# Kernel tuning notes

Hardware: AMD Instinct MI355X
Metric: run time of the kernel (lower is better)

Reference implementation:

```python
import jax, jax.numpy as jnp
import numpy as np

N = 50000        # nodes
E = 800000       # edges (avg degree 16)
F_IN = 128       # in_channels
HID = 32         # hidden_channels per head
H = 8            # heads
DH = HID * H     # 256, concat dim
NC = {'TL': 12, 'YL': 30, 'TS': 60, 'TZ': 120}
NEG_SLOPE = 0.2  # PyG GATConv default


def setup_inputs() -> dict:
    key = jax.random.key(0)
    ks = jax.random.split(key, 40)
    rn = lambda k, s, sc=0.1: jax.random.normal(k, s, jnp.float32) * sc
    inp = {}
    inp['x'] = jax.random.normal(ks[0], (N, F_IN), jnp.float32)
    inp['edge_index'] = jax.random.randint(ks[1], (2, E), 0, N, dtype=jnp.int64)
    # conv1: in -> H x HID (concat)
    inp['W1'] = rn(ks[2], (F_IN, DH)); inp['a1s'] = rn(ks[3], (H, HID)); inp['a1d'] = rn(ks[4], (H, HID)); inp['b1'] = jnp.zeros((DH,), jnp.float32)
    # conv2: DH -> H x HID (concat)
    inp['W2'] = rn(ks[5], (DH, DH)); inp['a2s'] = rn(ks[6], (H, HID)); inp['a2d'] = rn(ks[7], (H, HID)); inp['b2'] = jnp.zeros((DH,), jnp.float32)
    # task heads: DH -> C, heads=1, concat=False
    i = 8
    for t, c in NC.items():
        inp['W_' + t] = rn(ks[i], (DH, c)); i += 1
        inp['as_' + t] = rn(ks[i], (1, c)); i += 1
        inp['ad_' + t] = rn(ks[i], (1, c)); i += 1
        inp['b_' + t] = jnp.zeros((c,), jnp.float32)
    return inp


def gat_conv(x, src, dst, W, a_s, a_d, b, concat):
    """PyG-style GATConv (eval mode, self-loops already in src/dst)."""
    n = x.shape[0]
    heads, out_ch = a_s.shape
    h = (x @ W).reshape(n, heads, out_ch)                 # [N,H,C]
    alpha_s = jnp.einsum('nhc,hc->nh', h, a_s)            # [N,H]
    alpha_d = jnp.einsum('nhc,hc->nh', h, a_d)
    e = jax.nn.leaky_relu(alpha_s[src] + alpha_d[dst], NEG_SLOPE)   # [E,H]
    # numerically-stable segment softmax over incoming edges of each dst
    m = jax.ops.segment_max(e, dst, num_segments=n)
    ex = jnp.exp(e - m[dst])
    denom = jax.ops.segment_sum(ex, dst, num_segments=n)
    alpha = ex / (denom[dst] + 1e-16)                     # [E,H]
    out = jax.ops.segment_sum(alpha[:, :, None] * h[src], dst, num_segments=n)  # [N,H,C]
    out = out.reshape(n, heads * out_ch) if concat else out.mean(axis=1)
    return out + b


def reference(x, edge_index, W1, a1s, a1d, b1, W2, a2s, a2d, b2,
              W_TL, as_TL, ad_TL, b_TL, W_YL, as_YL, ad_YL, b_YL,
              W_TS, as_TS, ad_TS, b_TS, W_TZ, as_TZ, ad_TZ, b_TZ):
    n = x.shape[0]
    loop = jnp.arange(n, dtype=edge_index.dtype)
    src = jnp.concatenate([edge_index[0], loop])
    dst = jnp.concatenate([edge_index[1], loop])
    h = jax.nn.elu(gat_conv(x, src, dst, W1, a1s, a1d, b1, True))
    h = gat_conv(h, src, dst, W2, a2s, a2d, b2, True)
    tl = jax.nn.log_softmax(gat_conv(h, src, dst, W_TL, as_TL, ad_TL, b_TL, False), axis=1)
    yl = jax.nn.log_softmax(gat_conv(h, src, dst, W_YL, as_YL, ad_YL, b_YL, False), axis=1)
    ts = jax.nn.log_softmax(gat_conv(h, src, dst, W_TS, as_TS, ad_TS, b_TS, False), axis=1)
    tz = jax.nn.log_softmax(gat_conv(h, src, dst, W_TZ, as_TZ, ad_TZ, b_TZ, False), axis=1)
    return (tl, yl, ts, tz)
```

## Files before the change

### kernel.cpp

```cpp
#include <hip/hip_runtime.h>
#include <math.h>


#define NEG_SLOPE 0.2f

typedef short s8v __attribute__((ext_vector_type(8)));
typedef short s4v __attribute__((ext_vector_type(4)));
typedef float f4v __attribute__((ext_vector_type(4)));

__device__ __forceinline__ short f2bf(float x) {
    unsigned u = __float_as_uint(x);
    u += 0x7fffu + ((u >> 16) & 1u);
    return (short)(u >> 16);
}
__device__ __forceinline__ float bf2f(short b) {
    return __uint_as_float(((unsigned)(unsigned short)b) << 16);
}
__device__ __forceinline__ void split2(float x, short& h, short& l) {
    h = f2bf(x);
    l = f2bf(x - bf2f(h));
}
__device__ __forceinline__ float4 bf4_to_f4(s4v v) {
    return make_float4(bf2f(v[0]), bf2f(v[1]), bf2f(v[2]), bf2f(v[3]));
}
__device__ __forceinline__ float leaky(float x) {
    return fmaxf(x, NEG_SLOPE * x);
}


__global__ void init_kernel(int* __restrict__ deg, int* __restrict__ cursor, int n) {
    int i = blockIdx.x * blockDim.x + threadIdx.x;
    if (i < n) { deg[i] = 1; cursor[i] = 0; }
}

__global__ void count_kernel(const int* __restrict__ dst, int* __restrict__ deg, int E) {
    int i = blockIdx.x * blockDim.x + threadIdx.x;
    if (i < E) atomicAdd(&deg[dst[i]], 1);
}

__global__ __launch_bounds__(1024) void scan_kernel(const int* __restrict__ deg,
                                                    int* __restrict__ rowstart, int n) {
    __shared__ int wsum[16];
    __shared__ int carry_sh;
    int lane = threadIdx.x & 63, wv = threadIdx.x >> 6;
    if (threadIdx.x == 0) { carry_sh = 0; rowstart[0] = 0; }
    __syncthreads();
    for (int base = 0; base < n; base += 8192) {
        int vals[8];
        int sum = 0;
        int i0 = base + threadIdx.x * 8;
        #pragma unroll
        for (int j = 0; j < 8; ++j) {
            int i = i0 + j;
            int v = (i < n) ? ((deg[i] + 3) & ~3) : 0;
            sum += v;
            vals[j] = sum;
        }
        int incl = sum;
        #pragma unroll
        for (int off = 1; off < 64; off <<= 1) {
            int t = __shfl_up(incl, off);
            if (lane >= off) incl += t;
        }
        if (lane == 63) wsum[wv] = incl;
        __syncthreads();
        if (wv == 0) {
            int s = (lane < 16) ? wsum[lane] : 0;
            #pragma unroll
            for (int off = 1; off < 16; off <<= 1) {
                int t = __shfl_up(s, off);
                if (lane >= off) s += t;
            }
            if (lane < 16) wsum[lane] = s;
        }
        __syncthreads();
        int wexcl = (wv == 0) ? 0 : wsum[wv - 1];
        int excl = carry_sh + wexcl + (incl - sum);
        #pragma unroll
        for (int j = 0; j < 8; ++j) {
            int i = i0 + j;
            if (i < n) rowstart[i + 1] = excl + vals[j];
        }
        __syncthreads();
        if (threadIdx.x == 0) carry_sh += wsum[15];
        __syncthreads();
    }
}

__global__ void scatter_kernel(const int* __restrict__ src, const int* __restrict__ dst,
                               const int* __restrict__ rowstart, int* __restrict__ cursor,
                               int* __restrict__ csr, int E, int n) {
    int i = blockIdx.x * blockDim.x + threadIdx.x;
    if (i >= E + n) return;
    int s, d;
    if (i < E) { s = src[i]; d = dst[i]; }
    else       { s = d = i - E; }
    int p = atomicAdd(&cursor[d], 1);
    csr[rowstart[d] + p] = s;
}


__global__ void tobf_kernel(const float* __restrict__ A, short* __restrict__ Ah, int n4) {
    int i = blockIdx.x * blockDim.x + threadIdx.x;
    if (i >= n4) return;
    float4 v = ((const float4*)A)[i];
    s4v hv = {f2bf(v.x), f2bf(v.y), f2bf(v.z), f2bf(v.w)};
    ((s4v*)Ah)[i] = hv;
}

__global__ void split_bt_kernel(const float* __restrict__ B, short* __restrict__ Bh,
                                short* __restrict__ Bl, int K, int Nc, int kshift) {
    int idx = blockIdx.x * blockDim.x + threadIdx.x;
    if (idx >= Nc * K) return;
    int n = idx >> kshift;
    int k = idx & (K - 1);
    float v = B[(size_t)k * Nc + n];
    short h, l; split2(v, h, l);
    Bh[idx] = h;
    Bl[idx] = l;
}

__global__ void fold_alpha8_kernel(const float* __restrict__ W,
                                   const float* __restrict__ a_s, const float* __restrict__ a_d,
                                   short* __restrict__ Bth, short* __restrict__ Btl,
                                   int K, int Nfeat) {
    int idx = blockIdx.x * blockDim.x + threadIdx.x;
    if (idx >= K * 16) return;
    int j = idx / K, k = idx % K;
    int h = j & 7;
    const float* av = ((j < 8) ? a_s : a_d) + h * 32;
    const float* wp = W + (size_t)k * 256 + h * 32;
    float s = 0.f;
    #pragma unroll
    for (int c = 0; c < 32; ++c) s += wp[c] * av[c];
    short hi, lo; split2(s, hi, lo);
    size_t off = (size_t)(Nfeat + j) * K + k;
    Bth[off] = hi; Btl[off] = lo;
}

__global__ void fold_alpha4_kernel(const float* __restrict__ Wcat,
                                   const float* __restrict__ ascat, const float* __restrict__ adcat,
                                   short* __restrict__ Bth, short* __restrict__ Btl) {
    int idx = blockIdx.x * blockDim.x + threadIdx.x;
    if (idx >= 256 * 8) return;
    int j = idx >> 8, k = idx & 255;
    const int CO[4] = {0, 12, 44, 104};
    const int CL[4] = {12, 32, 60, 120};
    int t = j & 3;
    const float* av = ((j < 4) ? ascat : adcat) + CO[t];
    const float* wp = Wcat + (size_t)k * 224 + CO[t];
    float s = 0.f;
    for (int c = 0; c < CL[t]; ++c) s += wp[c] * av[c];
    short hi, lo; split2(s, hi, lo);
    size_t off = (size_t)(224 + j) * 256 + k;
    Bth[off] = hi; Btl[off] = lo;
}


#define MB 128
#define NB 64
#define KS 32

__global__ __launch_bounds__(256) void gemm_mfma_kernel(
        const short* __restrict__ Ah_g,
        const short* __restrict__ Bth_g, const short* __restrict__ Btl_g,
        short* __restrict__ Cb, int cb_stride,
        float* __restrict__ als, float* __restrict__ ald, int nsplit,
        int M, int K, int Nfeat, int NcExt) {
    __shared__ __align__(16) short Ah[MB][40];
    __shared__ __align__(16) short Bh[NB][40];
    __shared__ __align__(16) short Bl[NB][40];

    int t = threadIdx.x;
    int lane = t & 63, w = t >> 6;
    int quad = lane >> 4, l16 = lane & 15;
    int row0 = blockIdx.y * MB, col0 = blockIdx.x * NB;

    f4v acc[2][4];
    #pragma unroll
    for (int mt = 0; mt < 2; ++mt)
        #pragma unroll
        for (int nt = 0; nt < 4; ++nt)
            acc[mt][nt] = (f4v){0.f, 0.f, 0.f, 0.f};

    for (int k0 = 0; k0 < K; k0 += KS) {
        __syncthreads();
        #pragma unroll
        for (int i = 0; i < 2; ++i) {
            int u = i * 256 + t;
            int r = u >> 2, kk = (u & 3) * 8;
            int gr = row0 + r;
            s8v vh = {0, 0, 0, 0, 0, 0, 0, 0};
            if (gr < M) vh = *(const s8v*)(Ah_g + (size_t)gr * K + k0 + kk);
            *(s8v*)&Ah[r][kk] = vh;
        }
        {
            int n = t >> 2, kk = (t & 3) * 8;
            int gc = col0 + n;
            s8v vh = {0, 0, 0, 0, 0, 0, 0, 0};
            s8v vl = {0, 0, 0, 0, 0, 0, 0, 0};
            if (gc < NcExt) {
                vh = *(const s8v*)(Bth_g + (size_t)gc * K + k0 + kk);
                vl = *(const s8v*)(Btl_g + (size_t)gc * K + k0 + kk);
            }
            *(s8v*)&Bh[n][kk] = vh;
            *(s8v*)&Bl[n][kk] = vl;
        }
        __syncthreads();

        int kb = quad * 8;
        s8v a_f[2], b_h[4], b_l[4];
        #pragma unroll
        for (int mt = 0; mt < 2; ++mt) {
            int r = w * 32 + mt * 16 + l16;
            a_f[mt] = *(const s8v*)&Ah[r][kb];
        }
        #pragma unroll
        for (int nt = 0; nt < 4; ++nt) {
            int c = nt * 16 + l16;
            b_h[nt] = *(const s8v*)&Bh[c][kb];
            b_l[nt] = *(const s8v*)&Bl[c][kb];
        }
        #pragma unroll
        for (int mt = 0; mt < 2; ++mt)
            #pragma unroll
            for (int nt = 0; nt < 4; ++nt) {
                acc[mt][nt] = __builtin_amdgcn_mfma_f32_16x16x32_bf16(
                    a_f[mt], b_h[nt], acc[mt][nt], 0, 0, 0);
                acc[mt][nt] = __builtin_amdgcn_mfma_f32_16x16x32_bf16(
                    a_f[mt], b_l[nt], acc[mt][nt], 0, 0, 0);
            }
    }

    #pragma unroll
    for (int mt = 0; mt < 2; ++mt) {
        #pragma unroll
        for (int nt = 0; nt < 4; ++nt) {
            int gc = col0 + nt * 16 + l16;
            if (gc >= NcExt) continue;
            #pragma unroll
            for (int r = 0; r < 4; ++r) {
                int gr = row0 + w * 32 + mt * 16 + quad * 4 + r;
                if (gr >= M) continue;
                float v = acc[mt][nt][r];
                if (gc < Nfeat) {
                    Cb[(size_t)gr * cb_stride + gc] = f2bf(v);
                } else {
                    int j = gc - Nfeat;
                    if (j < nsplit)            als[(size_t)gr * nsplit + j] = v;
                    else if (j < 2 * nsplit)   ald[(size_t)gr * nsplit + (j - nsplit)] = v;
                }
            }
        }
    }
}


__global__ __launch_bounds__(256) void gat_gather_kernel(
        const short* __restrict__ hb,
        const float* __restrict__ als, const float* __restrict__ ald,
        const int* __restrict__ rowstart, const int* __restrict__ csr,
        const float* __restrict__ bias, short* __restrict__ oh, int n, int elu) {
    int wid  = blockIdx.x * 4 + (threadIdx.x >> 6);
    int lane = threadIdx.x & 63;
    if (wid >= n) return;
    int row = rowstart[wid];
    int pdeg = rowstart[wid + 1] - row;
    int hp = lane >> 3;
    int ch = lane * 4;
    int ph = lane & 7;
    const int* cp = csr + row;
    float aldv = ald[(size_t)wid * 8 + ph];

    float4 acc = {0.f, 0.f, 0.f, 0.f};
    float wsum = 0.f;
    for (int base = 0; base < pdeg; base += 64) {
        int cnt = min(pdeg - base, 64);
        int idxv = -1;
        if (lane < cnt) idxv = cp[base + lane];
        int e = 0;
        for (; e + 8 <= cnt; e += 8) {
            int si[8];
            #pragma unroll
            for (int i = 0; i < 8; ++i) {
                int r = __builtin_amdgcn_readlane(idxv, e + i);
                si[i] = r < 0 ? 0 : r;
            }
            s4v hv[8];
            #pragma unroll
            for (int i = 0; i < 8; ++i)
                hv[i] = *(const s4v*)(hb + (size_t)si[i] * 256 + ch);
            int sprod = __shfl(idxv, e + (lane >> 3));
            int sp = sprod < 0 ? 0 : sprod;
            float wall = __expf(leaky(als[(size_t)sp * 8 + ph] + aldv));
            if (sprod < 0) wall = 0.f;
            float w[8];
            #pragma unroll
            for (int i = 0; i < 8; ++i) w[i] = __shfl(wall, i * 8 + hp);
            #pragma unroll
            for (int i = 0; i < 8; ++i) {
                float4 h = bf4_to_f4(hv[i]);
                acc.x += w[i] * h.x; acc.y += w[i] * h.y;
                acc.z += w[i] * h.z; acc.w += w[i] * h.w;
                wsum += w[i];
            }
        }
        if (e < cnt) {
            int si[4];
            #pragma unroll
            for (int i = 0; i < 4; ++i) {
                int r = __builtin_amdgcn_readlane(idxv, e + i);
                si[i] = r < 0 ? 0 : r;
            }
            s4v hv[4];
            #pragma unroll
            for (int i = 0; i < 4; ++i)
                hv[i] = *(const s4v*)(hb + (size_t)si[i] * 256 + ch);
            int sprod = __shfl(idxv, e + ((lane >> 3) & 3));
            int sp = sprod < 0 ? 0 : sprod;
            float wall = __expf(leaky(als[(size_t)sp * 8 + ph] + aldv));
            if (sprod < 0) wall = 0.f;
            float w[4];
            #pragma unroll
            for (int i = 0; i < 4; ++i) w[i] = __shfl(wall, i * 8 + hp);
            #pragma unroll
            for (int i = 0; i < 4; ++i) {
                float4 h = bf4_to_f4(hv[i]);
                acc.x += w[i] * h.x; acc.y += w[i] * h.y;
                acc.z += w[i] * h.z; acc.w += w[i] * h.w;
                wsum += w[i];
            }
        }
    }
    float inv = 1.f / (wsum + 1e-16f);
    float4 b4 = *(const float4*)(bias + ch);
    float v[4] = {acc.x * inv + b4.x, acc.y * inv + b4.y,
                  acc.z * inv + b4.z, acc.w * inv + b4.w};
    if (elu) {
        #pragma unroll
        for (int j = 0; j < 4; ++j)
            v[j] = (v[j] > 0.f) ? v[j] : __expf(v[j]) - 1.f;
    }
    s4v hvo = {f2bf(v[0]), f2bf(v[1]), f2bf(v[2]), f2bf(v[3])};
    *(s4v*)(oh + (size_t)wid * 256 + ch) = hvo;
}


__global__ void pack_w_kernel(const float* __restrict__ wTL, const float* __restrict__ wYL,
                              const float* __restrict__ wTS, const float* __restrict__ wTZ,
                              const float* __restrict__ bTL, const float* __restrict__ bYL,
                              const float* __restrict__ bTS, const float* __restrict__ bTZ,
                              const float* __restrict__ asTL, const float* __restrict__ asYL,
                              const float* __restrict__ asTS, const float* __restrict__ asTZ,
                              const float* __restrict__ adTL, const float* __restrict__ adYL,
                              const float* __restrict__ adTS, const float* __restrict__ adTZ,
                              float* __restrict__ Wcat, float* __restrict__ bcat,
                              float* __restrict__ ascat, float* __restrict__ adcat) {
    int idx = blockIdx.x * blockDim.x + threadIdx.x;
    if (idx < 256 * 224) {
        int r = idx / 224, c = idx % 224;
        float v = 0.f;
        if (c < 12)       v = wTL[r * 12 + c];
        else if (c < 42)  v = wYL[r * 30 + (c - 12)];
        else if (c < 44)  v = 0.f;
        else if (c < 104) v = wTS[r * 60 + (c - 44)];
        else              v = wTZ[r * 120 + (c - 104)];
        Wcat[idx] = v;
    }
    if (idx < 224) {
        float b = 0.f, as_ = 0.f, ad_ = 0.f;
        if (idx < 12)       { b = bTL[idx];       as_ = asTL[idx];       ad_ = adTL[idx]; }
        else if (idx < 42)  { b = bYL[idx - 12];  as_ = asYL[idx - 12];  ad_ = adYL[idx - 12]; }
        else if (idx < 44)  { }
        else if (idx < 104) { b = bTS[idx - 44];  as_ = asTS[idx - 44];  ad_ = adTS[idx - 44]; }
        else                { b = bTZ[idx - 104]; as_ = asTZ[idx - 104]; ad_ = adTZ[idx - 104]; }
        bcat[idx]  = b;
        ascat[idx] = as_;
        adcat[idx] = ad_;
    }
}


__device__ __forceinline__ float sel4(int t, float v0, float v1, float v2, float v3) {
    return (t == 0) ? v0 : (t == 1) ? v1 : (t == 2) ? v2 : v3;
}

__global__ __launch_bounds__(256) void task_gather_ls_kernel(
        const short* __restrict__ htb,
        const float* __restrict__ ast, const float* __restrict__ adt,
        const int* __restrict__ rowstart, const int* __restrict__ csr,
        const float* __restrict__ bcat, float* __restrict__ out, int n) {
    int wid  = blockIdx.x * 4 + (threadIdx.x >> 6);
    int lane = threadIdx.x & 63;
    if (wid >= n) return;
    int row = rowstart[wid];
    int pdeg = rowstart[wid + 1] - row;
    int ch0 = (lane < 56) ? lane * 4 : 0;
    int t = (lane < 3) ? 0 : (lane < 11) ? 1 : (lane < 26) ? 2 : 3;
    int pt = lane & 3;
    int COp = (t == 0) ? 0 : (t == 1) ? 12 : (t == 2) ? 44 : 104;
    int COr = (t == 0) ? 0 : (t == 1) ? 12 : (t == 2) ? 42 : 102;
    int CLr = (t == 0) ? 12 : (t == 1) ? 30 : (t == 2) ? 60 : 120;
    bool valj[4];
    #pragma unroll
    for (int j = 0; j < 4; ++j)
        valj[j] = (unsigned)(ch0 + j - COp) < (unsigned)CLr;

    const int* cp = csr + row;
    float adtv = adt[(size_t)wid * 4 + pt];

    float acc[4] = {0.f, 0.f, 0.f, 0.f};
    float wsv = 0.f;
    for (int base = 0; base < pdeg; base += 64) {
        int cnt = min(pdeg - base, 64);
        int idxv = -1;
        if (lane < cnt) idxv = cp[base + lane];
        int e = 0;
        for (; e + 8 <= cnt; e += 8) {
            int si[8];
            #pragma unroll
            for (int i = 0; i < 8; ++i) {
                int r = __builtin_amdgcn_readlane(idxv, e + i);
                si[i] = r < 0 ? 0 : r;
            }
            s4v hv[8];
            #pragma unroll
            for (int i = 0; i < 8; ++i)
                hv[i] = *(const s4v*)(htb + (size_t)si[i] * 224 + ch0);
            int sprod = __shfl(idxv, e + (lane >> 3));
            int sp = sprod < 0 ? 0 : sprod;
            float wall = __expf(leaky(ast[(size_t)sp * 4 + pt] + adtv));
            if (sprod < 0) wall = 0.f;
            float w[8];
            #pragma unroll
            for (int i = 0; i < 8; ++i) w[i] = __shfl(wall, i * 8 + t);
            #pragma unroll
            for (int i = 0; i < 8; ++i) {
                float4 h = bf4_to_f4(hv[i]);
                acc[0] += w[i] * h.x; acc[1] += w[i] * h.y;
                acc[2] += w[i] * h.z; acc[3] += w[i] * h.w;
                wsv += w[i];
            }
        }
        if (e < cnt) {
            int si[4];
            #pragma unroll
            for (int i = 0; i < 4; ++i) {
                int r = __builtin_amdgcn_readlane(idxv, e + i);
                si[i] = r < 0 ? 0 : r;
            }
            s4v hv[4];
            #pragma unroll
            for (int i = 0; i < 4; ++i)
                hv[i] = *(const s4v*)(htb + (size_t)si[i] * 224 + ch0);
            int sprod = __shfl(idxv, e + ((lane >> 3) & 3));
            int sp = sprod < 0 ? 0 : sprod;
            float wall = __expf(leaky(ast[(size_t)sp * 4 + pt] + adtv));
            if (sprod < 0) wall = 0.f;
            float w[4];
            #pragma unroll
            for (int i = 0; i < 4; ++i) w[i] = __shfl(wall, i * 8 + t);
            #pragma unroll
            for (int i = 0; i < 4; ++i) {
                float4 h = bf4_to_f4(hv[i]);
                acc[0] += w[i] * h.x; acc[1] += w[i] * h.y;
                acc[2] += w[i] * h.z; acc[3] += w[i] * h.w;
                wsv += w[i];
            }
        }
    }
    float inv = 1.f / (wsv + 1e-16f);

    float vout[4];
    float m = -1e30f;
    #pragma unroll
    for (int j = 0; j < 4; ++j) {
        float v = 0.f;
        if (valj[j]) { v = acc[j] * inv + bcat[ch0 + j]; m = fmaxf(m, v); }
        vout[j] = v;
    }
    float m0 = (t == 0) ? m : -1e30f;
    float m1 = (t == 1) ? m : -1e30f;
    float m2 = (t == 2) ? m : -1e30f;
    float m3 = (t == 3) ? m : -1e30f;
    #pragma unroll
    for (int off = 1; off < 64; off <<= 1) {
        m0 = fmaxf(m0, __shfl_xor(m0, off));
        m1 = fmaxf(m1, __shfl_xor(m1, off));
        m2 = fmaxf(m2, __shfl_xor(m2, off));
        m3 = fmaxf(m3, __shfl_xor(m3, off));
    }
    float mt = sel4(t, m0, m1, m2, m3);
    float sacc = 0.f;
    #pragma unroll
    for (int j = 0; j < 4; ++j)
        if (valj[j]) sacc += __expf(vout[j] - mt);
    float s0 = (t == 0) ? sacc : 0.f;
    float s1 = (t == 1) ? sacc : 0.f;
    float s2 = (t == 2) ? sacc : 0.f;
    float s3 = (t == 3) ? sacc : 0.f;
    #pragma unroll
    for (int off = 1; off < 64; off <<= 1) {
        s0 += __shfl_xor(s0, off);
        s1 += __shfl_xor(s1, off);
        s2 += __shfl_xor(s2, off);
        s3 += __shfl_xor(s3, off);
    }
    float st = sel4(t, s0, s1, s2, s3);
    float lse = mt + __logf(st);
    #pragma unroll
    for (int j = 0; j < 4; ++j)
        if (valj[j])
            out[(size_t)COr * n + (size_t)wid * CLr + (ch0 + j - COp)] = vout[j] - lse;
}


extern "C" void kernel_launch(void* const* d_in, const int* in_sizes, int n_in,
                              void* d_out, int out_size, void* d_ws, size_t ws_size,
                              hipStream_t stream) {
    const float* x   = (const float*)d_in[0];
    const int*   ei  = (const int*)d_in[1];
    const float* W1  = (const float*)d_in[2];
    const float* a1s = (const float*)d_in[3];
    const float* a1d = (const float*)d_in[4];
    const float* b1  = (const float*)d_in[5];
    const float* W2  = (const float*)d_in[6];
    const float* a2s = (const float*)d_in[7];
    const float* a2d = (const float*)d_in[8];
    const float* b2  = (const float*)d_in[9];
    const float* W_TL = (const float*)d_in[10]; const float* as_TL = (const float*)d_in[11];
    const float* ad_TL = (const float*)d_in[12]; const float* b_TL = (const float*)d_in[13];
    const float* W_YL = (const float*)d_in[14]; const float* as_YL = (const float*)d_in[15];
    const float* ad_YL = (const float*)d_in[16]; const float* b_YL = (const float*)d_in[17];
    const float* W_TS = (const float*)d_in[18]; const float* as_TS = (const float*)d_in[19];
    const float* ad_TS = (const float*)d_in[20]; const float* b_TS = (const float*)d_in[21];
    const float* W_TZ = (const float*)d_in[22]; const float* as_TZ = (const float*)d_in[23];
    const float* ad_TZ = (const float*)d_in[24]; const float* b_TZ = (const float*)d_in[25];

    const int N = in_sizes[0] / 128;
    const int E = in_sizes[1] / 2;
    const int* e_src = ei;
    const int* e_dst = ei + E;
    const int M4 = E + 4 * N;

    float* ws = (float*)d_ws;
    float* B1   = ws;
    float* B2   = B1 + (size_t)N * 256;
    float* B3   = B2 + (size_t)N * 256;
    float* as1  = B3 + (size_t)N * 256;
    float* ad1  = as1 + (size_t)N * 8;
    float* as2  = ad1 + (size_t)N * 8;
    float* ad2  = as2 + (size_t)N * 8;
    float* ast  = ad2 + (size_t)N * 8;
    float* adt  = ast + (size_t)N * 4;
    float* Wcat = adt + (size_t)N * 4;
    float* bcat = Wcat + 256 * 224;
    float* ascat = bcat + 224;
    float* adcat = ascat + 224;
    int* deg      = (int*)(adcat + 224);
    int* rowstart = deg + N;
    int* cursor   = rowstart + (N + 4);
    int* csr      = cursor + N;
    uintptr_t wsp = (uintptr_t)(csr + M4);
    wsp = (wsp + 15) & ~(uintptr_t)15;
    short* W1h = (short*)wsp;
    short* W1l = W1h + 272 * 128;
    short* W2h = W1l + 272 * 128;
    short* W2l = W2h + 272 * 256;
    short* Wth = W2l + 272 * 256;
    short* Wtl = Wth + 232 * 256;
    short* Xh  = (short*)B1;
    short* Sh  = (short*)B1;
    short* Th  = (short*)B1;
    short* h1b = (short*)B2;
    short* h2b = (short*)B2;
    short* htb = (short*)B2;

    float* out = (float*)d_out;

    const int B = 256;
    init_kernel<<<(N + B - 1) / B, B, 0, stream>>>(deg, cursor, N);
    count_kernel<<<(E + B - 1) / B, B, 0, stream>>>(e_dst, deg, E);
    scan_kernel<<<1, 1024, 0, stream>>>(deg, rowstart, N);
    hipMemsetAsync(csr, 0xFF, (size_t)M4 * sizeof(int), stream);
    scatter_kernel<<<(E + N + B - 1) / B, B, 0, stream>>>(e_src, e_dst, rowstart, cursor, csr, E, N);
    pack_w_kernel<<<(256 * 224 + B - 1) / B, B, 0, stream>>>(W_TL, W_YL, W_TS, W_TZ,
        b_TL, b_YL, b_TS, b_TZ, as_TL, as_YL, as_TS, as_TZ, ad_TL, ad_YL, ad_TS, ad_TZ,
        Wcat, bcat, ascat, adcat);
    split_bt_kernel<<<(256 * 128 + B - 1) / B, B, 0, stream>>>(W1, W1h, W1l, 128, 256, 7);
    split_bt_kernel<<<(256 * 256 + B - 1) / B, B, 0, stream>>>(W2, W2h, W2l, 256, 256, 8);
    split_bt_kernel<<<(224 * 256 + B - 1) / B, B, 0, stream>>>(Wcat, Wth, Wtl, 256, 224, 8);
    fold_alpha8_kernel<<<(128 * 16 + B - 1) / B, B, 0, stream>>>(W1, a1s, a1d, W1h, W1l, 128, 256);
    fold_alpha8_kernel<<<(256 * 16 + B - 1) / B, B, 0, stream>>>(W2, a2s, a2d, W2h, W2l, 256, 256);
    fold_alpha4_kernel<<<(256 * 8 + B - 1) / B, B, 0, stream>>>(Wcat, ascat, adcat, Wth, Wtl);
    tobf_kernel<<<((N * 128 / 4) + B - 1) / B, B, 0, stream>>>(x, Xh, N * 128 / 4);
    {
        dim3 g((272 + NB - 1) / NB, (N + MB - 1) / MB);
        gemm_mfma_kernel<<<g, 256, 0, stream>>>(Xh, W1h, W1l, h1b, 256,
                                                as1, ad1, 8, N, 128, 256, 272);
    }
    gat_gather_kernel<<<(N + 3) / 4, 256, 0, stream>>>(h1b, as1, ad1, rowstart, csr, b1, Sh, N, 1);
    {
        dim3 g((272 + NB - 1) / NB, (N + MB - 1) / MB);
        gemm_mfma_kernel<<<g, 256, 0, stream>>>(Sh, W2h, W2l, h2b, 256,
                                                as2, ad2, 8, N, 256, 256, 272);
    }
    gat_gather_kernel<<<(N + 3) / 4, 256, 0, stream>>>(h2b, as2, ad2, rowstart, csr, b2, Th, N, 0);
    {
        dim3 g((232 + NB - 1) / NB, (N + MB - 1) / MB);
        gemm_mfma_kernel<<<g, 256, 0, stream>>>(Th, Wth, Wtl, htb, 224,
                                                ast, adt, 4, N, 256, 224, 232);
    }
    task_gather_ls_kernel<<<(N + 3) / 4, 256, 0, stream>>>(htb, ast, adt, rowstart, csr, bcat, out, N);
}
```

Baseline: 595.2 us.

## Use 16-byte row loads in gather kernels, split edges across half-waves

Both gather kernels now have each lane load 8 bf16 features (16 bytes) rather than 4. The two half-waves each handle alternate edges, and their partial sums are combined at the end with a cross-lane shuffle. To let the task-head gather use aligned 8-wide loads, the concatenated task weights are re-laid out with each head starting on an 8-aligned column, and the intermediate buffer uses a 256 stride. The intent is fewer, wider memory transactions and more edges in flight per wave. The cost is the final reduction and half the lanes sitting idle in the epilogue.

```diff
diff --git a/kernel.cpp b/kernel.cpp
--- a/kernel.cpp
+++ b/kernel.cpp
@@ -19,9 +19,6 @@
 __device__ __forceinline__ void split2(float x, short& h, short& l) {
     h = f2bf(x);
     l = f2bf(x - bf2f(h));
-}
-__device__ __forceinline__ float4 bf4_to_f4(s4v v) {
-    return make_float4(bf2f(v[0]), bf2f(v[1]), bf2f(v[2]), bf2f(v[3]));
 }
 __device__ __forceinline__ float leaky(float x) {
     return fmaxf(x, NEG_SLOPE * x);
@@ -144,15 +141,15 @@
     int idx = blockIdx.x * blockDim.x + threadIdx.x;
     if (idx >= 256 * 8) return;
     int j = idx >> 8, k = idx & 255;
-    const int CO[4] = {0, 12, 44, 104};
-    const int CL[4] = {12, 32, 60, 120};
+    const int CO[4] = {0, 16, 48, 112};
+    const int CL[4] = {12, 30, 60, 120};
     int t = j & 3;
     const float* av = ((j < 4) ? ascat : adcat) + CO[t];
-    const float* wp = Wcat + (size_t)k * 224 + CO[t];
+    const float* wp = Wcat + (size_t)k * 232 + CO[t];
     float s = 0.f;
     for (int c = 0; c < CL[t]; ++c) s += wp[c] * av[c];
     short hi, lo; split2(s, hi, lo);
-    size_t off = (size_t)(224 + j) * 256 + k;
+    size_t off = (size_t)(232 + j) * 256 + k;
     Bth[off] = hi; Btl[off] = lo;
 }
 
@@ -266,13 +263,15 @@
     if (wid >= n) return;
     int row = rowstart[wid];
     int pdeg = rowstart[wid + 1] - row;
-    int hp = lane >> 3;
-    int ch = lane * 4;
-    int ph = lane & 7;
+    int ep  = lane >> 5;
+    int cb  = lane & 31;
+    int ch8 = cb * 8;
+    int hd  = cb >> 2;
+    int ph  = lane & 7;
     const int* cp = csr + row;
     float aldv = ald[(size_t)wid * 8 + ph];
 
-    float4 acc = {0.f, 0.f, 0.f, 0.f};
+    float acc[8] = {0.f, 0.f, 0.f, 0.f, 0.f, 0.f, 0.f, 0.f};
     float wsum = 0.f;
     for (int base = 0; base < pdeg; base += 64) {
         int cnt = min(pdeg - base, 64);
@@ -280,69 +279,77 @@
         if (lane < cnt) idxv = cp[base + lane];
         int e = 0;
         for (; e + 8 <= cnt; e += 8) {
-            int si[8];
-            #pragma unroll
-            for (int i = 0; i < 8; ++i) {
-                int r = __builtin_amdgcn_readlane(idxv, e + i);
-                si[i] = r < 0 ? 0 : r;
-            }
-            s4v hv[8];
-            #pragma unroll
-            for (int i = 0; i < 8; ++i)
-                hv[i] = *(const s4v*)(hb + (size_t)si[i] * 256 + ch);
+            int sg[8];
+            #pragma unroll
+            for (int g = 0; g < 8; ++g) {
+                int r = __builtin_amdgcn_readlane(idxv, e + g);
+                sg[g] = r < 0 ? 0 : r;
+            }
+            s8v hv[4];
+            #pragma unroll
+            for (int k = 0; k < 4; ++k) {
+                int ssel = ep ? sg[2 * k + 1] : sg[2 * k];
+                hv[k] = *(const s8v*)(hb + (size_t)ssel * 256 + ch8);
+            }
             int sprod = __shfl(idxv, e + (lane >> 3));
             int sp = sprod < 0 ? 0 : sprod;
             float wall = __expf(leaky(als[(size_t)sp * 8 + ph] + aldv));
             if (sprod < 0) wall = 0.f;
-            float w[8];
-            #pragma unroll
-            for (int i = 0; i < 8; ++i) w[i] = __shfl(wall, i * 8 + hp);
-            #pragma unroll
-            for (int i = 0; i < 8; ++i) {
-                float4 h = bf4_to_f4(hv[i]);
-                acc.x += w[i] * h.x; acc.y += w[i] * h.y;
-                acc.z += w[i] * h.z; acc.w += w[i] * h.w;
-                wsum += w[i];
+            #pragma unroll
+            for (int k = 0; k < 4; ++k) {
+                float wk = __shfl(wall, (2 * k + ep) * 8 + hd);
+                #pragma unroll
+                for (int j = 0; j < 8; ++j)
+                    acc[j] += wk * bf2f(hv[k][j]);
+                wsum += wk;
             }
         }
         if (e < cnt) {
-            int si[4];
-            #pragma unroll
-            for (int i = 0; i < 4; ++i) {
-                int r = __builtin_amdgcn_readlane(idxv, e + i);
-                si[i] = r < 0 ? 0 : r;
-            }
-            s4v hv[4];
-            #pragma unroll
-            for (int i = 0; i < 4; ++i)
-                hv[i] = *(const s4v*)(hb + (size_t)si[i] * 256 + ch);
+            int sg[4];
+            #pragma unroll
+            for (int g = 0; g < 4; ++g) {
+                int r = __builtin_amdgcn_readlane(idxv, e + g);
+                sg[g] = r < 0 ? 0 : r;
+            }
+            s8v hv[2];
+            #pragma unroll
+            for (int k = 0; k < 2; ++k) {
+                int ssel = ep ? sg[2 * k + 1] : sg[2 * k];
+                hv[k] = *(const s8v*)(hb + (size_t)ssel * 256 + ch8);
+            }
             int sprod = __shfl(idxv, e + ((lane >> 3) & 3));
             int sp = sprod < 0 ? 0 : sprod;
             float wall = __expf(leaky(als[(size_t)sp * 8 + ph] + aldv));
             if (sprod < 0) wall = 0.f;
-            float w[4];
-            #pragma unroll
-            for (int i = 0; i < 4; ++i) w[i] = __shfl(wall, i * 8 + hp);
-            #pragma unroll
-            for (int i = 0; i < 4; ++i) {
-                float4 h = bf4_to_f4(hv[i]);
-                acc.x += w[i] * h.x; acc.y += w[i] * h.y;
-                acc.z += w[i] * h.z; acc.w += w[i] * h.w;
-                wsum += w[i];
-            }
-        }
-    }
+            #pragma unroll
+            for (int k = 0; k < 2; ++k) {
+                float wk = __shfl(wall, (2 * k + ep) * 8 + hd);
+                #pragma unroll
+                for (int j = 0; j < 8; ++j)
+                    acc[j] += wk * bf2f(hv[k][j]);
+                wsum += wk;
+            }
+        }
+    }
+    wsum += __shfl_xor(wsum, 32);
+    #pragma unroll
+    for (int j = 0; j < 8; ++j)
+        acc[j] += __shfl_xor(acc[j], 32);
     float inv = 1.f / (wsum + 1e-16f);
-    float4 b4 = *(const float4*)(bias + ch);
-    float v[4] = {acc.x * inv + b4.x, acc.y * inv + b4.y,
-                  acc.z * inv + b4.z, acc.w * inv + b4.w};
-    if (elu) {
-        #pragma unroll
-        for (int j = 0; j < 4; ++j)
-            v[j] = (v[j] > 0.f) ? v[j] : __expf(v[j]) - 1.f;
-    }
-    s4v hvo = {f2bf(v[0]), f2bf(v[1]), f2bf(v[2]), f2bf(v[3])};
-    *(s4v*)(oh + (size_t)wid * 256 + ch) = hvo;
+    if (lane < 32) {
+        float4 b0 = *(const float4*)(bias + ch8);
+        float4 b1 = *(const float4*)(bias + ch8 + 4);
+        float bb[8] = {b0.x, b0.y, b0.z, b0.w, b1.x, b1.y, b1.z, b1.w};
+        short vv[8];
+        #pragma unroll
+        for (int j = 0; j < 8; ++j) {
+            float v = acc[j] * inv + bb[j];
+            if (elu) v = (v > 0.f) ? v : __expf(v) - 1.f;
+            vv[j] = f2bf(v);
+        }
+        s8v hvo = {vv[0], vv[1], vv[2], vv[3], vv[4], vv[5], vv[6], vv[7]};
+        *(s8v*)(oh + (size_t)wid * 256 + ch8) = hvo;
+    }
 }
 
 
@@ -357,23 +364,21 @@
                               float* __restrict__ Wcat, float* __restrict__ bcat,
                               float* __restrict__ ascat, float* __restrict__ adcat) {
     int idx = blockIdx.x * blockDim.x + threadIdx.x;
-    if (idx < 256 * 224) {
-        int r = idx / 224, c = idx % 224;
+    if (idx < 256 * 232) {
+        int r = idx / 232, c = idx % 232;
         float v = 0.f;
-        if (c < 12)       v = wTL[r * 12 + c];
-        else if (c < 42)  v = wYL[r * 30 + (c - 12)];
-        else if (c < 44)  v = 0.f;
-        else if (c < 104) v = wTS[r * 60 + (c - 44)];
-        else              v = wTZ[r * 120 + (c - 104)];
+        if (c < 12)                    v = wTL[r * 12 + c];
+        else if (c >= 16 && c < 46)    v = wYL[r * 30 + (c - 16)];
+        else if (c >= 48 && c < 108)   v = wTS[r * 60 + (c - 48)];
+        else if (c >= 112 && c < 232)  v = wTZ[r * 120 + (c - 112)];
         Wcat[idx] = v;
     }
-    if (idx < 224) {
+    if (idx < 232) {
         float b = 0.f, as_ = 0.f, ad_ = 0.f;
-        if (idx < 12)       { b = bTL[idx];       as_ = asTL[idx];       ad_ = adTL[idx]; }
-        else if (idx < 42)  { b = bYL[idx - 12];  as_ = asYL[idx - 12];  ad_ = adYL[idx - 12]; }
-        else if (idx < 44)  { }
-        else if (idx < 104) { b = bTS[idx - 44];  as_ = asTS[idx - 44];  ad_ = adTS[idx - 44]; }
-        else                { b = bTZ[idx - 104]; as_ = asTZ[idx - 104]; ad_ = adTZ[idx - 104]; }
+        if (idx < 12)                    { b = bTL[idx];       as_ = asTL[idx];       ad_ = adTL[idx]; }
+        else if (idx >= 16 && idx < 46)  { b = bYL[idx - 16];  as_ = asYL[idx - 16];  ad_ = adYL[idx - 16]; }
+        else if (idx >= 48 && idx < 108) { b = bTS[idx - 48];  as_ = asTS[idx - 48];  ad_ = adTS[idx - 48]; }
+        else if (idx >= 112)             { b = bTZ[idx - 112]; as_ = asTZ[idx - 112]; ad_ = adTZ[idx - 112]; }
         bcat[idx]  = b;
         ascat[idx] = as_;
         adcat[idx] = ad_;
@@ -395,21 +400,25 @@
     if (wid >= n) return;
     int row = rowstart[wid];
     int pdeg = rowstart[wid + 1] - row;
-    int ch0 = (lane < 56) ? lane * 4 : 0;
-    int t = (lane < 3) ? 0 : (lane < 11) ? 1 : (lane < 26) ? 2 : 3;
+    int ep  = lane >> 5;
+    int cb  = lane & 31;
+    int cbr = (cb <= 28) ? cb : 0;
+    int ch8 = cbr * 8;
+    int t = (ch8 >= 112) ? 3 : (ch8 >= 48) ? 2 : (ch8 >= 16) ? 1 : 0;
+    int pe = (lane & 31) >> 2;
     int pt = lane & 3;
-    int COp = (t == 0) ? 0 : (t == 1) ? 12 : (t == 2) ? 44 : 104;
+    int COp = (t == 0) ? 0 : (t == 1) ? 16 : (t == 2) ? 48 : 112;
     int COr = (t == 0) ? 0 : (t == 1) ? 12 : (t == 2) ? 42 : 102;
     int CLr = (t == 0) ? 12 : (t == 1) ? 30 : (t == 2) ? 60 : 120;
-    bool valj[4];
-    #pragma unroll
-    for (int j = 0; j < 4; ++j)
-        valj[j] = (unsigned)(ch0 + j - COp) < (unsigned)CLr;
+    bool valj[8];
+    #pragma unroll
+    for (int j = 0; j < 8; ++j)
+        valj[j] = (cb <= 28) && ((unsigned)(ch8 + j - COp) < (unsigned)CLr);
 
     const int* cp = csr + row;
     float adtv = adt[(size_t)wid * 4 + pt];
 
-    float acc[4] = {0.f, 0.f, 0.f, 0.f};
+    float acc[8] = {0.f, 0.f, 0.f, 0.f, 0.f, 0.f, 0.f, 0.f};
     float wsv = 0.f;
     for (int base = 0; base < pdeg; base += 64) {
         int cnt = min(pdeg - base, 64);
@@ -417,66 +426,73 @@
         if (lane < cnt) idxv = cp[base + lane];
         int e = 0;
         for (; e + 8 <= cnt; e += 8) {
-            int si[8];
-            #pragma unroll
-            for (int i = 0; i < 8; ++i) {
-                int r = __builtin_amdgcn_readlane(idxv, e + i);
-                si[i] = r < 0 ? 0 : r;
-            }
-            s4v hv[8];
-            #pragma unroll
-            for (int i = 0; i < 8; ++i)
-                hv[i] = *(const s4v*)(htb + (size_t)si[i] * 224 + ch0);
-            int sprod = __shfl(idxv, e + (lane >> 3));
+            int sg[8];
+            #pragma unroll
+            for (int g = 0; g < 8; ++g) {
+                int r = __builtin_amdgcn_readlane(idxv, e + g);
+                sg[g] = r < 0 ? 0 : r;
+            }
+            s8v hv[4];
+            #pragma unroll
+            for (int k = 0; k < 4; ++k) {
+                int ssel = ep ? sg[2 * k + 1] : sg[2 * k];
+                hv[k] = *(const s8v*)(htb + (size_t)ssel * 256 + ch8);
+            }
+            int sprod = __shfl(idxv, e + pe);
             int sp = sprod < 0 ? 0 : sprod;
             float wall = __expf(leaky(ast[(size_t)sp * 4 + pt] + adtv));
             if (sprod < 0) wall = 0.f;
-            float w[8];
-            #pragma unroll
-            for (int i = 0; i < 8; ++i) w[i] = __shfl(wall, i * 8 + t);
-            #pragma unroll
-            for (int i = 0; i < 8; ++i) {
-                float4 h = bf4_to_f4(hv[i]);
-                acc[0] += w[i] * h.x; acc[1] += w[i] * h.y;
-                acc[2] += w[i] * h.z; acc[3] += w[i] * h.w;
-                wsv += w[i];
+            #pragma unroll
+            for (int k = 0; k < 4; ++k) {
+                float wk = __shfl(wall, (2 * k + ep) * 4 + t);
+                #pragma unroll
+                for (int j = 0; j < 8; ++j)
+                    acc[j] += wk * bf2f(hv[k][j]);
+                wsv += wk;
             }
         }
         if (e < cnt) {
-            int si[4];
-            #pragma unroll
-            for (int i = 0; i < 4; ++i) {
-                int r = __builtin_amdgcn_readlane(idxv, e + i);
-                si[i] = r < 0 ? 0 : r;
-            }
-            s4v hv[4];
-            #pragma unroll
-            for (int i = 0; i < 4; ++i)
-                hv[i] = *(const s4v*)(htb + (size_t)si[i] * 224 + ch0);
-            int sprod = __shfl(idxv, e + ((lane >> 3) & 3));
+            int sg[4];
+            #pragma unroll
+            for (int g = 0; g < 4; ++g) {
+                int r = __builtin_amdgcn_readlane(idxv, e + g);
+                sg[g] = r < 0 ? 0 : r;
+            }
+            s8v hv[2];
+            #pragma unroll
+            for (int k = 0; k < 2; ++k) {
+                int ssel = ep ? sg[2 * k + 1] : sg[2 * k];
+                hv[k] = *(const s8v*)(htb + (size_t)ssel * 256 + ch8);
+            }
+            int sprod = __shfl(idxv, e + (pe & 3));
             int sp = sprod < 0 ? 0 : sprod;
             float wall = __expf(leaky(ast[(size_t)sp * 4 + pt] + adtv));
             if (sprod < 0) wall = 0.f;
-            float w[4];
-            #pragma unroll
-            for (int i = 0; i < 4; ++i) w[i] = __shfl(wall, i * 8 + t);
-            #pragma unroll
-            for (int i = 0; i < 4; ++i) {
-                float4 h = bf4_to_f4(hv[i]);
-                acc[0] += w[i] * h.x; acc[1] += w[i] * h.y;
-                acc[2] += w[i] * h.z; acc[3] += w[i] * h.w;
-                wsv += w[i];
-            }
-        }
-    }
+            #pragma unroll
+            for (int k = 0; k < 2; ++k) {
+                float wk = __shfl(wall, (2 * k + ep) * 4 + t);
+                #pragma unroll
+                for (int j = 0; j < 8; ++j)
+                    acc[j] += wk * bf2f(hv[k][j]);
+                wsv += wk;
+            }
+        }
+    }
+    wsv += __shfl_xor(wsv, 32);
+    #pragma unroll
+    for (int j = 0; j < 8; ++j)
+        acc[j] += __shfl_xor(acc[j], 32);
     float inv = 1.f / (wsv + 1e-16f);
 
-    float vout[4];
+    float4 bc0 = *(const float4*)(bcat + ch8);
+    float4 bc1 = *(const float4*)(bcat + ch8 + 4);
+    float bb[8] = {bc0.x, bc0.y, bc0.z, bc0.w, bc1.x, bc1.y, bc1.z, bc1.w};
+    float vout[8];
     float m = -1e30f;
     #pragma unroll
-    for (int j = 0; j < 4; ++j) {
+    for (int j = 0; j < 8; ++j) {
         float v = 0.f;
-        if (valj[j]) { v = acc[j] * inv + bcat[ch0 + j]; m = fmaxf(m, v); }
+        if (valj[j]) { v = acc[j] * inv + bb[j]; m = fmaxf(m, v); }
         vout[j] = v;
     }
     float m0 = (t == 0) ? m : -1e30f;
@@ -492,9 +508,11 @@
     }
     float mt = sel4(t, m0, m1, m2, m3);
     float sacc = 0.f;
-    #pragma unroll
-    for (int j = 0; j < 4; ++j)
-        if (valj[j]) sacc += __expf(vout[j] - mt);
+    if (ep == 0) {
+        #pragma unroll
+        for (int j = 0; j < 8; ++j)
+            if (valj[j]) sacc += __expf(vout[j] - mt);
+    }
     float s0 = (t == 0) ? sacc : 0.f;
     float s1 = (t == 1) ? sacc : 0.f;
     float s2 = (t == 2) ? sacc : 0.f;
@@ -508,10 +526,12 @@
     }
     float st = sel4(t, s0, s1, s2, s3);
     float lse = mt + __logf(st);
-    #pragma unroll
-    for (int j = 0; j < 4; ++j)
-        if (valj[j])
-            out[(size_t)COr * n + (size_t)wid * CLr + (ch0 + j - COp)] = vout[j] - lse;
+    if (ep == 0) {
+        #pragma unroll
+        for (int j = 0; j < 8; ++j)
+            if (valj[j])
+                out[(size_t)COr * n + (size_t)wid * CLr + (ch8 + j - COp)] = vout[j] - lse;
+    }
 }
 
 
@@ -554,10 +574,10 @@
     float* ast  = ad2 + (size_t)N * 8;
     float* adt  = ast + (size_t)N * 4;
     float* Wcat = adt + (size_t)N * 4;
-    float* bcat = Wcat + 256 * 224;
-    float* ascat = bcat + 224;
-    float* adcat = ascat + 224;
-    int* deg      = (int*)(adcat + 224);
+    float* bcat = Wcat + 256 * 232;
+    float* ascat = bcat + 240;
+    float* adcat = ascat + 240;
+    int* deg      = (int*)(adcat + 240);
     int* rowstart = deg + N;
     int* cursor   = rowstart + (N + 4);
     int* csr      = cursor + N;
@@ -568,7 +588,7 @@
     short* W2h = W1l + 272 * 128;
     short* W2l = W2h + 272 * 256;
     short* Wth = W2l + 272 * 256;
-    short* Wtl = Wth + 232 * 256;
+    short* Wtl = Wth + 240 * 256;
     short* Xh  = (short*)B1;
     short* Sh  = (short*)B1;
     short* Th  = (short*)B1;
@@ -584,12 +604,12 @@
     scan_kernel<<<1, 1024, 0, stream>>>(deg, rowstart, N);
     hipMemsetAsync(csr, 0xFF, (size_t)M4 * sizeof(int), stream);
     scatter_kernel<<<(E + N + B - 1) / B, B, 0, stream>>>(e_src, e_dst, rowstart, cursor, csr, E, N);
-    pack_w_kernel<<<(256 * 224 + B - 1) / B, B, 0, stream>>>(W_TL, W_YL, W_TS, W_TZ,
+    pack_w_kernel<<<(256 * 232 + B - 1) / B, B, 0, stream>>>(W_TL, W_YL, W_TS, W_TZ,
         b_TL, b_YL, b_TS, b_TZ, as_TL, as_YL, as_TS, as_TZ, ad_TL, ad_YL, ad_TS, ad_TZ,
         Wcat, bcat, ascat, adcat);
     split_bt_kernel<<<(256 * 128 + B - 1) / B, B, 0, stream>>>(W1, W1h, W1l, 128, 256, 7);
     split_bt_kernel<<<(256 * 256 + B - 1) / B, B, 0, stream>>>(W2, W2h, W2l, 256, 256, 8);
-    split_bt_kernel<<<(224 * 256 + B - 1) / B, B, 0, stream>>>(Wcat, Wth, Wtl, 256, 224, 8);
+    split_bt_kernel<<<(232 * 256 + B - 1) / B, B, 0, stream>>>(Wcat, Wth, Wtl, 256, 232, 8);
     fold_alpha8_kernel<<<(128 * 16 + B - 1) / B, B, 0, stream>>>(W1, a1s, a1d, W1h, W1l, 128, 256);
     fold_alpha8_kernel<<<(256 * 16 + B - 1) / B, B, 0, stream>>>(W2, a2s, a2d, W2h, W2l, 256, 256);
     fold_alpha4_kernel<<<(256 * 8 + B - 1) / B, B, 0, stream>>>(Wcat, ascat, adcat, Wth, Wtl);
@@ -607,9 +627,9 @@
     }
     gat_gather_kernel<<<(N + 3) / 4, 256, 0, stream>>>(h2b, as2, ad2, rowstart, csr, b2, Th, N, 0);
     {
-        dim3 g((232 + NB - 1) / NB, (N + MB - 1) / MB);
-        gemm_mfma_kernel<<<g, 256, 0, stream>>>(Th, Wth, Wtl, htb, 224,
-                                                ast, adt, 4, N, 256, 224, 232);
+        dim3 g((240 + NB - 1) / NB, (N + MB - 1) / MB);
+        gemm_mfma_kernel<<<g, 256, 0, stream>>>(Th, Wth, Wtl, htb, 256,
+                                                ast, adt, 4, N, 256, 232, 240);
     }
     task_gather_ls_kernel<<<(N + 3) / 4, 256, 0, stream>>>(htb, ast, adt, rowstart, csr, bcat, out, N);
 }
```

Result: slower. 616.5 us (+3.6%).
